# Performance work log

Measured on AMD Instinct MI355X. Metric: run time of the kernel, lower is better.

## Reference

```python
import jax, jax.numpy as jnp
import numpy as np

N, D = 12288, 128
T = 0.07  # temperature from __init__ default


def setup_inputs() -> dict:
    key = jax.random.key(0)
    x = jax.random.normal(key, (N, D), dtype=jnp.float32)
    # L2-normalize rows (this loss is defined on unit-norm embeddings;
    # keeps exp(sim / 0.07) finite in fp32 while preserving the exact math).
    x = x / jnp.linalg.norm(x, axis=-1, keepdims=True)
    return {"x": x}


def reference(x):
    # x: [N, D] -> sim: [N, N]
    sim = jnp.matmul(x, x.T) / T
    # faithful to torch: exp -> sum over last dim -> log -> mean (no LSE stabilization)
    return jnp.mean(jnp.log(jnp.sum(jnp.exp(sim), axis=-1)))
```

## Files before the change

kernel.cpp:

```cpp
#include <hip/hip_runtime.h>
#include <hip/hip_bf16.h>

#define NROWS 12288
#define DDIM  128
#define NT    96
#define CHUNK 12
#define NBLK  432

typedef __bf16 bf16x8 __attribute__((ext_vector_type(8)));
typedef float  f32x4  __attribute__((ext_vector_type(4)));

__device__ __forceinline__ unsigned short f2bf(float f) {
    union { float f; unsigned u; } a; a.f = f;
    unsigned r = a.u + 0x7fffu + ((a.u >> 16) & 1u);
    return (unsigned short)(r >> 16);
}

__global__ void convert_kernel(const float* __restrict__ x, unsigned short* __restrict__ xbT,
                               float* __restrict__ rowsum, float* __restrict__ out) {
    int gid = blockIdx.x * 256 + threadIdx.x;
    int e = gid << 3;
    float4 v0 = *(const float4*)(x + e);
    float4 v1 = *(const float4*)(x + e + 4);
    uint4 o;
    o.x = (unsigned)f2bf(v0.x) | ((unsigned)f2bf(v0.y) << 16);
    o.y = (unsigned)f2bf(v0.z) | ((unsigned)f2bf(v0.w) << 16);
    o.z = (unsigned)f2bf(v1.x) | ((unsigned)f2bf(v1.y) << 16);
    o.w = (unsigned)f2bf(v1.z) | ((unsigned)f2bf(v1.w) << 16);
    int r = gid >> 4;
    int c = gid & 15;
    size_t off = ((size_t)((r >> 4) * 4 + (c >> 2)) * 64 + (c & 3) * 16 + (r & 15)) * 8;
    *(uint4*)(xbT + off) = o;
    if (gid < NROWS) rowsum[gid] = 0.f;
    if (gid == 0) out[0] = 0.f;
}

__global__ __launch_bounds__(256, 2) void gemm_exp_rowsum(
    const unsigned short* __restrict__ xbT, float* __restrict__ rowsum)
{
    __shared__ float csumS[CHUNK * 128];

    const int tid = threadIdx.x;

    int rem = blockIdx.x, bi = 0;
    for (;;) {
        int nch = (NT - bi + CHUNK - 1) / CHUNK;
        if (rem < nch) break;
        rem -= nch; ++bi;
    }
    const int jt0 = bi + rem * CHUNK;
    const int ntiles = min(CHUNK, NT - jt0);
    const int i0 = bi * 128;

    for (int k = tid; k < CHUNK * 128; k += 256) csumS[k] = 0.f;

    const int wave = tid >> 6, lane = tid & 63;
    const int m16 = lane & 15, q = lane >> 4;
    const int wr = wave >> 1, wc = wave & 1;

    bf16x8 af[4][4];
    #pragma unroll
    for (int mi = 0; mi < 4; ++mi) {
        int arb = bi * 8 + wr * 4 + mi;
        #pragma unroll
        for (int ks = 0; ks < 4; ++ks)
            af[mi][ks] = *(const bf16x8*)(xbT + ((size_t)(arb * 4 + ks) * 64 + lane) * 8);
    }
    __syncthreads();

    const float SCALE = 20.609929155556625f;

    f32x4 rp4[4];
    #pragma unroll
    for (int mi = 0; mi < 4; ++mi) rp4[mi] = (f32x4){0.f, 0.f, 0.f, 0.f};

    for (int t = 0; t < ntiles; ++t) {
        const int jt = jt0 + t;

        const unsigned short* bbase = xbT + (size_t)((jt * 8 + wc * 4) * 4) * 64 * 8;
        bf16x8 bfr[4][4];
        #pragma unroll
        for (int ks = 0; ks < 4; ++ks)
            #pragma unroll
            for (int ni = 0; ni < 4; ++ni)
                bfr[ks][ni] = *(const bf16x8*)(bbase + ((size_t)(ni * 4 + ks) * 64 + lane) * 8);

        f32x4 acc[4][4] = {};
        #pragma unroll
        for (int ks = 0; ks < 4; ++ks)
            #pragma unroll
            for (int mi = 0; mi < 4; ++mi)
                #pragma unroll
                for (int ni = 0; ni < 4; ++ni)
                    acc[mi][ni] = __builtin_amdgcn_mfma_f32_16x16x32_bf16(
                        af[mi][ks], bfr[ks][ni], acc[mi][ni], 0, 0, 0);

        f32x4 cp4[4];
        #pragma unroll
        for (int ni = 0; ni < 4; ++ni) cp4[ni] = (f32x4){0.f, 0.f, 0.f, 0.f};

        #pragma unroll
        for (int mi = 0; mi < 4; ++mi)
            #pragma unroll
            for (int ni = 0; ni < 4; ++ni) {
                f32x4 sv = acc[mi][ni] * SCALE;
                f32x4 ev;
                ev[0] = __builtin_amdgcn_exp2f(sv[0]);
                ev[1] = __builtin_amdgcn_exp2f(sv[1]);
                ev[2] = __builtin_amdgcn_exp2f(sv[2]);
                ev[3] = __builtin_amdgcn_exp2f(sv[3]);
                rp4[mi] += ev;
                cp4[ni] += ev;
            }

        if (jt != bi) {
            #pragma unroll
            for (int ni = 0; ni < 4; ++ni) {
                float s = (cp4[ni][0] + cp4[ni][1]) + (cp4[ni][2] + cp4[ni][3]);
                s += __shfl_xor(s, 16);
                s += __shfl_xor(s, 32);
                if (q == 0) atomicAdd(&csumS[t * 128 + wc * 64 + ni * 16 + m16], s);
            }
        }
    }

    #pragma unroll
    for (int mi = 0; mi < 4; ++mi)
        #pragma unroll
        for (int r = 0; r < 4; ++r) {
            float s = rp4[mi][r];
            s += __shfl_xor(s, 1);
            s += __shfl_xor(s, 2);
            s += __shfl_xor(s, 4);
            s += __shfl_xor(s, 8);
            if (m16 == 0) atomicAdd(&rowsum[i0 + wr * 64 + mi * 16 + q * 4 + r], s);
        }

    __syncthreads();
    for (int k = tid; k < ntiles * 128; k += 256) {
        float v = csumS[k];
        if (v != 0.f) atomicAdd(&rowsum[jt0 * 128 + k], v);
    }
}

__global__ void finalize_kernel(const float* __restrict__ rowsum, float* __restrict__ out) {
    __shared__ float red[4];
    int gid = blockIdx.x * 256 + threadIdx.x;
    float lg = __logf(rowsum[gid]);
    #pragma unroll
    for (int off = 1; off < 64; off <<= 1)
        lg += __shfl_xor(lg, off);
    const int wv = threadIdx.x >> 6, ln = threadIdx.x & 63;
    if (ln == 0) red[wv] = lg;
    __syncthreads();
    if (threadIdx.x == 0)
        atomicAdd(out, (red[0] + red[1] + red[2] + red[3]) * (1.0f / (float)NROWS));
}

extern "C" void kernel_launch(void* const* d_in, const int* in_sizes, int n_in,
                              void* d_out, int out_size, void* d_ws, size_t ws_size,
                              hipStream_t stream) {
    const float* x = (const float*)d_in[0];
    float* out = (float*)d_out;

    float* rowsum = (float*)d_ws;
    unsigned short* xbT = (unsigned short*)((char*)d_ws + NROWS * sizeof(float));

    convert_kernel<<<dim3((NROWS * DDIM) / (8 * 256)), dim3(256), 0, stream>>>(x, xbT, rowsum, out);
    gemm_exp_rowsum<<<dim3(NBLK), dim3(256), 0, stream>>>(xbT, rowsum);
    finalize_kernel<<<dim3(NROWS / 256), dim3(256), 0, stream>>>(rowsum, out);
}
```

Measured before the change: 98.22 us.

## Balance triangular tile work evenly across 512 blocks with row-crossing flushes

```diff
diff --git a/kernel.cpp b/kernel.cpp
--- a/kernel.cpp
+++ b/kernel.cpp
@@ -4,8 +4,9 @@
 #define NROWS 12288
 #define DDIM  128
 #define NT    96
-#define CHUNK 12
-#define NBLK  432
+#define NTILE 4656
+#define NBLK  512
+#define MAXT  10
 
 typedef __bf16 bf16x8 __attribute__((ext_vector_type(8)));
 typedef float  f32x4  __attribute__((ext_vector_type(4)));
@@ -38,34 +39,37 @@
 __global__ __launch_bounds__(256, 2) void gemm_exp_rowsum(
     const unsigned short* __restrict__ xbT, float* __restrict__ rowsum)
 {
-    __shared__ float csumS[CHUNK * 128];
+    __shared__ float csumS[MAXT * 128];
+    __shared__ int jtArr[MAXT];
 
     const int tid = threadIdx.x;
+    const int g0 = (blockIdx.x * NTILE) >> 9;
+    const int g1 = ((blockIdx.x + 1) * NTILE) >> 9;
+    const int nt = g1 - g0;
 
-    int rem = blockIdx.x, bi = 0;
-    for (;;) {
-        int nch = (NT - bi + CHUNK - 1) / CHUNK;
-        if (rem < nch) break;
-        rem -= nch; ++bi;
-    }
-    const int jt0 = bi + rem * CHUNK;
-    const int ntiles = min(CHUNK, NT - jt0);
-    const int i0 = bi * 128;
+    int bi = 0, rem = g0;
+    while (rem >= NT - bi) { rem -= NT - bi; ++bi; }
+    int jt = bi + rem;
+    const int bi0 = bi, jt0 = jt;
 
-    for (int k = tid; k < CHUNK * 128; k += 256) csumS[k] = 0.f;
+    for (int k = tid; k < MAXT * 128; k += 256) csumS[k] = 0.f;
 
     const int wave = tid >> 6, lane = tid & 63;
     const int m16 = lane & 15, q = lane >> 4;
     const int wr = wave >> 1, wc = wave & 1;
 
     bf16x8 af[4][4];
-    #pragma unroll
-    for (int mi = 0; mi < 4; ++mi) {
-        int arb = bi * 8 + wr * 4 + mi;
-        #pragma unroll
-        for (int ks = 0; ks < 4; ++ks)
-            af[mi][ks] = *(const bf16x8*)(xbT + ((size_t)(arb * 4 + ks) * 64 + lane) * 8);
-    }
+    #define LOAD_AF() do {                                                       \
+        _Pragma("unroll")                                                        \
+        for (int mi = 0; mi < 4; ++mi) {                                         \
+            int arb = bi * 8 + wr * 4 + mi;                                      \
+            _Pragma("unroll")                                                    \
+            for (int ks = 0; ks < 4; ++ks)                                       \
+                af[mi][ks] = *(const bf16x8*)(xbT + ((size_t)(arb * 4 + ks) * 64 + lane) * 8); \
+        }                                                                        \
+    } while (0)
+
+    LOAD_AF();
     __syncthreads();
 
     const float SCALE = 20.609929155556625f;
@@ -74,9 +78,24 @@
     #pragma unroll
     for (int mi = 0; mi < 4; ++mi) rp4[mi] = (f32x4){0.f, 0.f, 0.f, 0.f};
 
-    for (int t = 0; t < ntiles; ++t) {
-        const int jt = jt0 + t;
+    #define FLUSH_RP() do {                                                      \
+        _Pragma("unroll")                                                        \
+        for (int mi = 0; mi < 4; ++mi) {                                         \
+            _Pragma("unroll")                                                    \
+            for (int r = 0; r < 4; ++r) {                                        \
+                float s = rp4[mi][r];                                            \
+                s += __shfl_xor(s, 1);                                           \
+                s += __shfl_xor(s, 2);                                           \
+                s += __shfl_xor(s, 4);                                           \
+                s += __shfl_xor(s, 8);                                           \
+                if (m16 == 0)                                                    \
+                    atomicAdd(&rowsum[bi * 128 + wr * 64 + mi * 16 + q * 4 + r], s); \
+            }                                                                    \
+            rp4[mi] = (f32x4){0.f, 0.f, 0.f, 0.f};                               \
+        }                                                                        \
+    } while (0)
 
+    for (int t = 0; t < nt; ++t) {
         const unsigned short* bbase = xbT + (size_t)((jt * 8 + wc * 4) * 4) * 64 * 8;
         bf16x8 bfr[4][4];
         #pragma unroll
@@ -122,25 +141,32 @@
                 if (q == 0) atomicAdd(&csumS[t * 128 + wc * 64 + ni * 16 + m16], s);
             }
         }
+
+        if (t + 1 < nt) {
+            ++jt;
+            if (jt == NT) {
+                FLUSH_RP();
+                ++bi; jt = bi;
+                LOAD_AF();
+            }
+        }
     }
+    FLUSH_RP();
 
-    #pragma unroll
-    for (int mi = 0; mi < 4; ++mi)
-        #pragma unroll
-        for (int r = 0; r < 4; ++r) {
-            float s = rp4[mi][r];
-            s += __shfl_xor(s, 1);
-            s += __shfl_xor(s, 2);
-            s += __shfl_xor(s, 4);
-            s += __shfl_xor(s, 8);
-            if (m16 == 0) atomicAdd(&rowsum[i0 + wr * 64 + mi * 16 + q * 4 + r], s);
+    if (tid == 0) {
+        int bb = bi0, jj = jt0;
+        for (int t = 0; t < nt; ++t) {
+            jtArr[t] = jj;
+            ++jj; if (jj == NT) { ++bb; jj = bb; }
         }
-
+    }
     __syncthreads();
-    for (int k = tid; k < ntiles * 128; k += 256) {
+    for (int k = tid; k < nt * 128; k += 256) {
         float v = csumS[k];
-        if (v != 0.f) atomicAdd(&rowsum[jt0 * 128 + k], v);
+        if (v != 0.f) atomicAdd(&rowsum[jtArr[k >> 7] * 128 + (k & 127)], v);
     }
+    #undef LOAD_AF
+    #undef FLUSH_RP
 }
 
 __global__ void finalize_kernel(const float* __restrict__ rowsum, float* __restrict__ out) {
```

After: 96.63 us. About the same (-1.6%).

## Stage A tile in LDS, software-pipeline B loads, replace atomics with partial buffers

Applied to the files above, without the earlier changes.

```diff
diff --git a/kernel.cpp b/kernel.cpp
--- a/kernel.cpp
+++ b/kernel.cpp
@@ -4,11 +4,15 @@
 #define NROWS 12288
 #define DDIM  128
 #define NT    96
-#define CHUNK 12
-#define NBLK  432
+#define CHUNK 10
+#define NBLK  510
 
 typedef __bf16 bf16x8 __attribute__((ext_vector_type(8)));
 typedef float  f32x4  __attribute__((ext_vector_type(4)));
+
+#define GLD_LDS(g, l) __builtin_amdgcn_global_load_lds(                      \
+    (const __attribute__((address_space(1))) void*)(g),                      \
+    (__attribute__((address_space(3))) void*)(l), 16, 0, 0)
 
 __device__ __forceinline__ unsigned short f2bf(float f) {
     union { float f; unsigned u; } a; a.f = f;
@@ -17,7 +21,7 @@
 }
 
 __global__ void convert_kernel(const float* __restrict__ x, unsigned short* __restrict__ xbT,
-                               float* __restrict__ rowsum, float* __restrict__ out) {
+                               float* __restrict__ out) {
     int gid = blockIdx.x * 256 + threadIdx.x;
     int e = gid << 3;
     float4 v0 = *(const float4*)(x + e);
@@ -29,15 +33,16 @@
     o.w = (unsigned)f2bf(v1.z) | ((unsigned)f2bf(v1.w) << 16);
     int r = gid >> 4;
     int c = gid & 15;
-    size_t off = ((size_t)((r >> 4) * 4 + (c >> 2)) * 64 + (c & 3) * 16 + (r & 15)) * 8;
+    int off = (((r >> 4) * 4 + (c >> 2)) * 64 + (c & 3) * 16 + (r & 15)) * 8;
     *(uint4*)(xbT + off) = o;
-    if (gid < NROWS) rowsum[gid] = 0.f;
     if (gid == 0) out[0] = 0.f;
 }
 
 __global__ __launch_bounds__(256, 2) void gemm_exp_rowsum(
-    const unsigned short* __restrict__ xbT, float* __restrict__ rowsum)
+    const unsigned short* __restrict__ xbT, float* __restrict__ rowpart,
+    float* __restrict__ colpart)
 {
+    __shared__ __align__(16) unsigned short Alds[128 * DDIM];
     __shared__ float csumS[CHUNK * 128];
 
     const int tid = threadIdx.x;
@@ -48,9 +53,9 @@
         if (rem < nch) break;
         rem -= nch; ++bi;
     }
-    const int jt0 = bi + rem * CHUNK;
+    const int chunkid = rem;
+    const int jt0 = bi + chunkid * CHUNK;
     const int ntiles = min(CHUNK, NT - jt0);
-    const int i0 = bi * 128;
 
     for (int k = tid; k < CHUNK * 128; k += 256) csumS[k] = 0.f;
 
@@ -58,13 +63,10 @@
     const int m16 = lane & 15, q = lane >> 4;
     const int wr = wave >> 1, wc = wave & 1;
 
-    bf16x8 af[4][4];
-    #pragma unroll
-    for (int mi = 0; mi < 4; ++mi) {
-        int arb = bi * 8 + wr * 4 + mi;
-        #pragma unroll
-        for (int ks = 0; ks < 4; ++ks)
-            af[mi][ks] = *(const bf16x8*)(xbT + ((size_t)(arb * 4 + ks) * 64 + lane) * 8);
+    #pragma unroll
+    for (int r8 = 0; r8 < 8; ++r8) {
+        int ch = r8 * 256 + wave * 64;
+        GLD_LDS(xbT + bi * 16384 + (ch + lane) * 8, Alds + ch * 8);
     }
     __syncthreads();
 
@@ -73,27 +75,43 @@
     f32x4 rp4[4];
     #pragma unroll
     for (int mi = 0; mi < 4; ++mi) rp4[mi] = (f32x4){0.f, 0.f, 0.f, 0.f};
+
+    #define LOAD_BKS(dst, jtv, ks) do {                                          \
+        int bb = ((jtv) * 8 + wc * 4);                                           \
+        _Pragma("unroll")                                                        \
+        for (int ni = 0; ni < 4; ++ni)                                           \
+            dst[ni] = *(const bf16x8*)(xbT + (((bb + ni) * 4 + (ks)) * 64 + lane) * 8); \
+    } while (0)
+
+    #define MFMA_KS(ks, bfr) do {                                                \
+        bf16x8 afk[4];                                                           \
+        _Pragma("unroll")                                                        \
+        for (int mi = 0; mi < 4; ++mi)                                           \
+            afk[mi] = *(const bf16x8*)(&Alds[(((wr * 4 + mi) * 4 + (ks)) * 64 + lane) * 8]); \
+        _Pragma("unroll")                                                        \
+        for (int mi = 0; mi < 4; ++mi)                                           \
+            _Pragma("unroll")                                                    \
+            for (int ni = 0; ni < 4; ++ni)                                       \
+                acc[mi][ni] = __builtin_amdgcn_mfma_f32_16x16x32_bf16(           \
+                    afk[mi], bfr[ni], acc[mi][ni], 0, 0, 0);                     \
+    } while (0)
+
+    bf16x8 bf0[4], bf1[4];
+    LOAD_BKS(bf0, jt0, 0);
 
     for (int t = 0; t < ntiles; ++t) {
         const int jt = jt0 + t;
-
-        const unsigned short* bbase = xbT + (size_t)((jt * 8 + wc * 4) * 4) * 64 * 8;
-        bf16x8 bfr[4][4];
-        #pragma unroll
-        for (int ks = 0; ks < 4; ++ks)
-            #pragma unroll
-            for (int ni = 0; ni < 4; ++ni)
-                bfr[ks][ni] = *(const bf16x8*)(bbase + ((size_t)(ni * 4 + ks) * 64 + lane) * 8);
+        const bool more = (t + 1 < ntiles);
 
         f32x4 acc[4][4] = {};
-        #pragma unroll
-        for (int ks = 0; ks < 4; ++ks)
-            #pragma unroll
-            for (int mi = 0; mi < 4; ++mi)
-                #pragma unroll
-                for (int ni = 0; ni < 4; ++ni)
-                    acc[mi][ni] = __builtin_amdgcn_mfma_f32_16x16x32_bf16(
-                        af[mi][ks], bfr[ks][ni], acc[mi][ni], 0, 0, 0);
+        LOAD_BKS(bf1, jt, 1);
+        MFMA_KS(0, bf0);
+        LOAD_BKS(bf0, jt, 2);
+        MFMA_KS(1, bf1);
+        LOAD_BKS(bf1, jt, 3);
+        MFMA_KS(2, bf0);
+        if (more) LOAD_BKS(bf0, jt + 1, 0);
+        MFMA_KS(3, bf1);
 
         f32x4 cp4[4];
         #pragma unroll
@@ -133,20 +151,34 @@
             s += __shfl_xor(s, 2);
             s += __shfl_xor(s, 4);
             s += __shfl_xor(s, 8);
-            if (m16 == 0) atomicAdd(&rowsum[i0 + wr * 64 + mi * 16 + q * 4 + r], s);
+            if (m16 == 0)
+                rowpart[(((bi * CHUNK + chunkid) * 2) + wc) * 128 + wr * 64 + mi * 16 + q * 4 + r] = s;
         }
 
     __syncthreads();
     for (int k = tid; k < ntiles * 128; k += 256) {
-        float v = csumS[k];
-        if (v != 0.f) atomicAdd(&rowsum[jt0 * 128 + k], v);
-    }
-}
-
-__global__ void finalize_kernel(const float* __restrict__ rowsum, float* __restrict__ out) {
+        int jt2 = jt0 + (k >> 7);
+        if (jt2 != bi) colpart[(bi * NT + jt2) * 128 + (k & 127)] = csumS[k];
+    }
+    #undef LOAD_BKS
+    #undef MFMA_KS
+}
+
+__global__ void finalize_kernel(const float* __restrict__ rowpart,
+                                const float* __restrict__ colpart,
+                                float* __restrict__ out) {
     __shared__ float red[4];
-    int gid = blockIdx.x * 256 + threadIdx.x;
-    float lg = __logf(rowsum[gid]);
+    int r = blockIdx.x * 256 + threadIdx.x;
+    int bj = r >> 7, c = r & 127;
+
+    float s = 0.f;
+    int nch = (NT - bj + CHUNK - 1) / CHUNK;
+    for (int ch = 0; ch < nch * 2; ++ch)
+        s += rowpart[(bj * CHUNK * 2 + ch) * 128 + c];
+    for (int b2 = 0; b2 < bj; ++b2)
+        s += colpart[(b2 * NT + bj) * 128 + c];
+
+    float lg = __logf(s);
     #pragma unroll
     for (int off = 1; off < 64; off <<= 1)
         lg += __shfl_xor(lg, off);
@@ -163,10 +195,11 @@
     const float* x = (const float*)d_in[0];
     float* out = (float*)d_out;
 
-    float* rowsum = (float*)d_ws;
-    unsigned short* xbT = (unsigned short*)((char*)d_ws + NROWS * sizeof(float));
-
-    convert_kernel<<<dim3((NROWS * DDIM) / (8 * 256)), dim3(256), 0, stream>>>(x, xbT, rowsum, out);
-    gemm_exp_rowsum<<<dim3(NBLK), dim3(256), 0, stream>>>(xbT, rowsum);
-    finalize_kernel<<<dim3(NROWS / 256), dim3(256), 0, stream>>>(rowsum, out);
-}
+    unsigned short* xbT = (unsigned short*)d_ws;
+    float* rowpart = (float*)((char*)d_ws + 3 * 1024 * 1024);
+    float* colpart = rowpart + NT * CHUNK * 2 * 128;
+
+    convert_kernel<<<dim3((NROWS * DDIM) / (8 * 256)), dim3(256), 0, stream>>>(x, xbT, out);
+    gemm_exp_rowsum<<<dim3(NBLK), dim3(256), 0, stream>>>(xbT, rowpart, colpart);
+    finalize_kernel<<<dim3(NROWS / 256), dim3(256), 0, stream>>>(rowpart, colpart, out);
+}
```

Result: slower. 113.9 us (+16.0%).
